# Performance work log

Measured on AMD Instinct MI355X. Metric: run time of the kernel, lower is better.

## Reference

```python
import jax, jax.numpy as jnp
import numpy as np
from jax import lax

TAU_REF_HOURS = 1.0
INIT_NOISE_SCALE = 0.01
MAX_GROWTH_RATE = 0.3
B, T, N, D = 2, 64, 512, 256


def setup_inputs() -> dict:
    key = jax.random.key(0)
    ks = jax.random.split(key, 8)
    return {
        "x": jax.random.normal(ks[0], (B, T, N, D), dtype=jnp.float32),
        "dt": jax.random.uniform(ks[1], (B, T), dtype=jnp.float32),
        "eps": jax.random.normal(ks[2], (B, T, N, D), dtype=jnp.float32),
        "u_raw_re": jax.random.normal(ks[3], (D, D), dtype=jnp.float32) * 0.02,
        "u_raw_im": jax.random.normal(ks[4], (D, D), dtype=jnp.float32) * 0.02,
        "lam_re": jax.random.normal(ks[5], (D,), dtype=jnp.float32) * 0.01,
        "lam_im": jax.random.normal(ks[6], (D,), dtype=jnp.float32) * 0.1,
        "noise_raw": jax.random.normal(ks[7], (D,), dtype=jnp.float32) * 0.02,
    }


def reference(x, dt, eps, u_raw_re, u_raw_im, lam_re, lam_im, noise_raw):
    # Unitary basis from QR of complex raw matrix (ComplexSVDTransform._unitary_from_raw)
    u, _ = jnp.linalg.qr(lax.complex(u_raw_re, u_raw_im))  # [D, D] complex

    # encode: x @ conj(u)
    x_enc = jnp.einsum("btnd,de->btne", x.astype(jnp.complex64), jnp.conj(u))

    # effective lambda: lam_re -> -softplus(-lam_re), clamped at -max_growth_rate
    lam_r = jnp.maximum(-jax.nn.softplus(-lam_re), -MAX_GROWTH_RATE)
    lam = lax.complex(lam_r, lam_im)  # [D]

    # continuous decay / forcing operators per (b, t, d)
    exp_arg = (dt / TAU_REF_HOURS)[..., None] * lam  # [B, T, D]
    decay = jnp.exp(exp_arg)
    lam_safe = lam + (1e-8 * jnp.sign(lam_r + 1e-12)).astype(lam.dtype)
    forcing = (decay - 1.0) / lam_safe  # expm1(arg)/lam_safe

    # SDE noise: eps * sqrt(dt) * softplus(noise_raw) * init_noise_scale
    dt_scale = jnp.sqrt(jnp.maximum(dt, 0.0))[:, :, None, None]  # [B,T,1,1]
    n_scale = jax.nn.softplus(noise_raw) * INIT_NOISE_SCALE  # [D]
    noise = eps.astype(jnp.complex64) * (dt_scale * n_scale).astype(jnp.complex64)

    # linear recurrence h_t = decay_t * h_{t-1} + forcing_t * x_enc_t + noise_t
    b_term = forcing[:, :, None, :] * x_enc + noise  # [B,T,N,D]
    a_term = jnp.broadcast_to(decay[:, :, None, :], b_term.shape)

    def combine(e1, e2):
        a1, b1 = e1
        a2, b2 = e2
        return (a2 * a1, a2 * b1 + b2)

    _, h = lax.associative_scan(combine, (a_term, b_term), axis=1)  # [B,T,N,D]

    # decode: h @ u
    y = jnp.einsum("btnd,de->btne", h, u)
    return jnp.stack([y.real, y.imag])  # [2,B,T,N,D] float32
```

## Files before the change

### kernel.cpp

```cpp
#include <hip/hip_runtime.h>
#include <math.h>

#define B_ 2
#define T_ 64
#define N_ 512
#define D_ 256
#define M_ (B_*T_*N_)
#define PLANE ((size_t)M_*D_)

typedef unsigned short u16;
typedef __attribute__((ext_vector_type(8))) short bf16x8;
typedef __attribute__((ext_vector_type(4))) float f32x4;

__device__ __forceinline__ u16 f2bf(float f) {
  union { float f; unsigned u; } cv; cv.f = f;
  unsigned u = cv.u;
  return (u16)((u + 0x7FFFu + ((u >> 16) & 1u)) >> 16);
}
__device__ __forceinline__ float bf2f(u16 h) {
  union { unsigned u; float f; } cv; cv.u = ((unsigned)h) << 16;
  return cv.f;
}

__device__ __forceinline__ float wredsum(float x) {
  x += __uint_as_float(__builtin_amdgcn_update_dpp(0u, __float_as_uint(x), 0x111, 0xf, 0xf, true));
  x += __uint_as_float(__builtin_amdgcn_update_dpp(0u, __float_as_uint(x), 0x112, 0xf, 0xf, true));
  x += __uint_as_float(__builtin_amdgcn_update_dpp(0u, __float_as_uint(x), 0x114, 0xf, 0xf, true));
  x += __uint_as_float(__builtin_amdgcn_update_dpp(0u, __float_as_uint(x), 0x118, 0xf, 0xf, true));
  x += __uint_as_float(__builtin_amdgcn_update_dpp(0u, __float_as_uint(x), 0x142, 0xa, 0xf, true));
  x += __uint_as_float(__builtin_amdgcn_update_dpp(0u, __float_as_uint(x), 0x143, 0xc, 0xf, true));
  return __uint_as_float(__builtin_amdgcn_readlane(__float_as_uint(x), 63));
}
__device__ __forceinline__ float lanebcast(float x, int l) {
  return __uint_as_float(__builtin_amdgcn_readlane(__float_as_uint(x), l));
}

template<int P>
__global__ __launch_bounds__(1024, 1) void qr_megastep(
    const float* __restrict__ ure_raw, const float* __restrict__ uim_raw,
    float2* __restrict__ A, float2* __restrict__ tau)
{
  const int tid = threadIdx.x, lane = tid & 63, w = tid >> 6;
  const int role = blockIdx.x;
  __shared__ float2 sv32[32][256];
  __shared__ float2 sfin[32][256];
  __shared__ float2 snA[2][256];
  __shared__ float2 snB[2][256];
  __shared__ float4 sscalAB[2];
  __shared__ float2 sg[2];
  __shared__ float2 stau32[32];
  __shared__ float2 stauOut[32];

  constexpr int J0P  = (P > 0) ? 32*(P-1) : 0;
  constexpr int RP   = 256 - J0P;
  constexpr int MCHP = (RP + 63) >> 6;
  constexpr int PIV  = (P == 0) ? 0 : 32;
  constexpr int J0W  = (P == 0) ? 0 : J0P;
  constexpr int RW   = 256 - J0W;
  constexpr int MCHW = (RW + 63) >> 6;

  if constexpr (P == 0) {
    if (role > 0) {
      const int c0 = 32*role;
      const int c = tid & 31, r0 = tid >> 5;
      #pragma unroll
      for (int r8 = 0; r8 < 8; ++r8) {
        int r = r0 + r8*32;
        A[(size_t)(c0+c)*D_ + r] = make_float2(ure_raw[(size_t)r*D_ + c0 + c],
                                               uim_raw[(size_t)r*D_ + c0 + c]);
      }
      return;
    }
  }

  float2 col[2][4];

  if constexpr (P > 0) {
    #pragma unroll
    for (int it = 0; it < 8; ++it) {
      int idx = it*1024 + tid;
      int c = idx >> 8, rr = idx & 255;
      float2 val = make_float2(0.f, 0.f);
      if (rr < RP) val = A[(size_t)(J0P+c)*D_ + J0P + rr];
      sv32[c][rr] = val;
    }
    if (tid < 32) stau32[tid] = tau[J0P + tid];
    const int c0 = (role > 0) ? 32*(P + role) : 32*P;
    #pragma unroll
    for (int lc = 0; lc < 2; ++lc) {
      int cg = c0 + 2*w + lc;
      #pragma unroll
      for (int m = 0; m < 4; ++m) {
        int rr = m*64 + lane;
        col[lc][m] = make_float2(0.f, 0.f);
        if (m < MCHP && rr < RP) col[lc][m] = A[(size_t)cg*D_ + J0P + rr];
      }
    }
    __syncthreads();

    #pragma unroll 4
    for (int jl = 0; jl < 32; ++jl) {
      float2 tt = stau32[jl];
      float2 v[4];
      { float2 rv = sv32[jl][lane];
        v[0] = (lane > jl) ? rv : ((lane == jl) ? make_float2(1.f, 0.f)
                                                : make_float2(0.f, 0.f)); }
      #pragma unroll
      for (int m = 1; m < 4; ++m) v[m] = sv32[jl][m*64 + lane];
      float wr[2], wi[2];
      #pragma unroll
      for (int lc = 0; lc < 2; ++lc) {
        wr[lc] = 0.f; wi[lc] = 0.f;
        #pragma unroll
        for (int m = 0; m < 4; ++m) {
          if (m < MCHP) {
            float2 a = col[lc][m];
            wr[lc] += v[m].x*a.x + v[m].y*a.y;
            wi[lc] += v[m].x*a.y - v[m].y*a.x;
          }
        }
      }
      #pragma unroll
      for (int lc = 0; lc < 2; ++lc) { wr[lc] = wredsum(wr[lc]);
                                       wi[lc] = wredsum(wi[lc]); }
      #pragma unroll
      for (int lc = 0; lc < 2; ++lc) {
        float fr = tt.x*wr[lc] + tt.y*wi[lc];
        float fi = tt.x*wi[lc] - tt.y*wr[lc];
        #pragma unroll
        for (int m = 0; m < 4; ++m) {
          if (m < MCHP) {
            col[lc][m].x -= fr*v[m].x - fi*v[m].y;
            col[lc][m].y -= fr*v[m].y + fi*v[m].x;
          }
        }
      }
    }

    if (role > 0) {
      #pragma unroll
      for (int lc = 0; lc < 2; ++lc) {
        int cg = 32*(P + role) + 2*w + lc;
        #pragma unroll
        for (int m = 0; m < 4; ++m) {
          int rr = m*64 + lane;
          if (m < MCHP && rr < RP) A[(size_t)cg*D_ + J0P + rr] = col[lc][m];
        }
      }
      return;
    }
    __syncthreads();
  } else {
    #pragma unroll
    for (int lc = 0; lc < 2; ++lc) {
      int cg = 2*w + lc;
      #pragma unroll
      for (int m = 0; m < 4; ++m) {
        int rr = m*64 + lane;
        col[lc][m] = make_float2(ure_raw[(size_t)rr*D_ + cg],
                                 uim_raw[(size_t)rr*D_ + cg]);
      }
    }
  }

  auto derive_pair = [&](float2 (&ca)[4], float2 (&cb)[4], int jlA, int buf) {
    const int prA = PIV + jlA, prB = prA + 1;
    float part = (lane > prA) ? (ca[0].x*ca[0].x + ca[0].y*ca[0].y) : 0.f;
    if (1 < MCHW) part += ca[1].x*ca[1].x + ca[1].y*ca[1].y;
    if (2 < MCHW) part += ca[2].x*ca[2].x + ca[2].y*ca[2].y;
    if (3 < MCHW) part += ca[3].x*ca[3].x + ca[3].y*ca[3].y;
    part = wredsum(part);
    float ar = lanebcast(ca[0].x, prA), ai = lanebcast(ca[0].y, prA);
    float trA, tiA, sr, si, btA;
    if (part == 0.f && ai == 0.f) {
      trA = tiA = sr = si = 0.f; btA = ar;
    } else {
      float nrm = sqrtf(ar*ar + ai*ai + part);
      btA = (ar >= 0.f) ? -nrm : nrm;
      trA = (btA - ar)/btA; tiA = -ai/btA;
      float dr = ar - btA, di = ai, dn = dr*dr + di*di;
      sr = dr/dn; si = -di/dn;
    }
    float2 vA[4];
    {
      float2 t0 = make_float2(ca[0].x*sr - ca[0].y*si, ca[0].x*si + ca[0].y*sr);
      vA[0] = (lane > prA) ? t0 : ((lane == prA) ? make_float2(1.f, 0.f)
                                                 : make_float2(0.f, 0.f));
    }
    vA[1] = make_float2(ca[1].x*sr - ca[1].y*si, ca[1].x*si + ca[1].y*sr);
    vA[2] = make_float2(ca[2].x*sr - ca[2].y*si, ca[2].x*si + ca[2].y*sr);
    vA[3] = make_float2(ca[3].x*sr - ca[3].y*si, ca[3].x*si + ca[3].y*sr);
    {
      float2 o0 = (lane < prA) ? ca[0]
                : ((lane == prA) ? make_float2(btA, 0.f) : vA[0]);
      sfin[jlA][lane] = o0;
      if (1 < MCHW) sfin[jlA][64 + lane]  = vA[1];
      if (2 < MCHW) sfin[jlA][128 + lane] = vA[2];
      if (3 < MCHW) sfin[jlA][192 + lane] = vA[3];
    }
    {
      float wr_ = vA[0].x*cb[0].x + vA[0].y*cb[0].y;
      float wi_ = vA[0].x*cb[0].y - vA[0].y*cb[0].x;
      if (1 < MCHW) { wr_ += vA[1].x*cb[1].x + vA[1].y*cb[1].y;
                      wi_ += vA[1].x*cb[1].y - vA[1].y*cb[1].x; }
      if (2 < MCHW) { wr_ += vA[2].x*cb[2].x + vA[2].y*cb[2].y;
                      wi_ += vA[2].x*cb[2].y - vA[2].y*cb[2].x; }
      if (3 < MCHW) { wr_ += vA[3].x*cb[3].x + vA[3].y*cb[3].y;
                      wi_ += vA[3].x*cb[3].y - vA[3].y*cb[3].x; }
      wr_ = wredsum(wr_); wi_ = wredsum(wi_);
      float fr = trA*wr_ + tiA*wi_;
      float fi = trA*wi_ - tiA*wr_;
      cb[0].x -= fr*vA[0].x - fi*vA[0].y; cb[0].y -= fr*vA[0].y + fi*vA[0].x;
      if (1 < MCHW) { cb[1].x -= fr*vA[1].x - fi*vA[1].y;
                      cb[1].y -= fr*vA[1].y + fi*vA[1].x; }
      if (2 < MCHW) { cb[2].x -= fr*vA[2].x - fi*vA[2].y;
                      cb[2].y -= fr*vA[2].y + fi*vA[2].x; }
      if (3 < MCHW) { cb[3].x -= fr*vA[3].x - fi*vA[3].y;
                      cb[3].y -= fr*vA[3].y + fi*vA[3].x; }
    }
    float partB = (lane > prB) ? (cb[0].x*cb[0].x + cb[0].y*cb[0].y) : 0.f;
    if (1 < MCHW) partB += cb[1].x*cb[1].x + cb[1].y*cb[1].y;
    if (2 < MCHW) partB += cb[2].x*cb[2].x + cb[2].y*cb[2].y;
    if (3 < MCHW) partB += cb[3].x*cb[3].x + cb[3].y*cb[3].y;
    partB = wredsum(partB);
    float br_ = lanebcast(cb[0].x, prB), bi_ = lanebcast(cb[0].y, prB);
    float trB, tiB, srB, siB, btB;
    if (partB == 0.f && bi_ == 0.f) {
      trB = tiB = srB = siB = 0.f; btB = br_;
    } else {
      float nrm = sqrtf(br_*br_ + bi_*bi_ + partB);
      btB = (br_ >= 0.f) ? -nrm : nrm;
      trB = (btB - br_)/btB; tiB = -bi_/btB;
      float dr = br_ - btB, di = bi_, dn = dr*dr + di*di;
      srB = dr/dn; siB = -di/dn;
    }
    float2 vB[4];
    {
      float2 t0 = make_float2(cb[0].x*srB - cb[0].y*siB, cb[0].x*siB + cb[0].y*srB);
      vB[0] = (lane > prB) ? t0 : ((lane == prB) ? make_float2(1.f, 0.f)
                                                 : make_float2(0.f, 0.f));
    }
    vB[1] = make_float2(cb[1].x*srB - cb[1].y*siB, cb[1].x*siB + cb[1].y*srB);
    vB[2] = make_float2(cb[2].x*srB - cb[2].y*siB, cb[2].x*siB + cb[2].y*srB);
    vB[3] = make_float2(cb[3].x*srB - cb[3].y*siB, cb[3].x*siB + cb[3].y*srB);
    {
      float2 o0 = (lane < prB) ? cb[0]
                : ((lane == prB) ? make_float2(btB, 0.f) : vB[0]);
      sfin[jlA+1][lane] = o0;
      if (1 < MCHW) sfin[jlA+1][64 + lane]  = vB[1];
      if (2 < MCHW) sfin[jlA+1][128 + lane] = vB[2];
      if (3 < MCHW) sfin[jlA+1][192 + lane] = vB[3];
    }
    float gr = vB[0].x*vA[0].x + vB[0].y*vA[0].y;
    float gi = vB[0].x*vA[0].y - vB[0].y*vA[0].x;
    if (1 < MCHW) { gr += vB[1].x*vA[1].x + vB[1].y*vA[1].y;
                    gi += vB[1].x*vA[1].y - vB[1].y*vA[1].x; }
    if (2 < MCHW) { gr += vB[2].x*vA[2].x + vB[2].y*vA[2].y;
                    gi += vB[2].x*vA[2].y - vB[2].y*vA[2].x; }
    if (3 < MCHW) { gr += vB[3].x*vA[3].x + vB[3].y*vA[3].y;
                    gi += vB[3].x*vA[3].y - vB[3].y*vA[3].x; }
    gr = wredsum(gr); gi = wredsum(gi);
    snA[buf][lane] = vA[0]; snA[buf][64+lane] = vA[1];
    snA[buf][128+lane] = vA[2]; snA[buf][192+lane] = vA[3];
    snB[buf][lane] = vB[0]; snB[buf][64+lane] = vB[1];
    snB[buf][128+lane] = vB[2]; snB[buf][192+lane] = vB[3];
    if (lane == 0) {
      sscalAB[buf] = make_float4(trA, tiA, trB, tiB);
      sg[buf] = make_float2(gr, gi);
      stauOut[jlA]   = make_float2(trA, tiA);
      stauOut[jlA+1] = make_float2(trB, tiB);
    }
  };

  if (w == 0) derive_pair(col[0], col[1], 0, 0);
  __syncthreads();

  #pragma unroll 1
  for (int m = 0; m < 15; ++m) {
    const int cur = m & 1, nxt = cur ^ 1;
    float2 vA0 = snA[cur][lane],       vA1 = snA[cur][64 + lane],
           vA2 = snA[cur][128 + lane], vA3 = snA[cur][192 + lane];
    float2 vB0 = snB[cur][lane],       vB1 = snB[cur][64 + lane],
           vB2 = snB[cur][128 + lane], vB3 = snB[cur][192 + lane];
    float4 sc = sscalAB[cur];
    float2 g  = sg[cur];
    #pragma unroll
    for (int lc = 0; lc < 2; ++lc) {
      int cl = 2*w + lc;
      if (cl > 2*m + 1) {
        float d1r, d1i, d2r, d2i;
        { float2 a = col[lc][0];
          d1r = vA0.x*a.x + vA0.y*a.y; d1i = vA0.x*a.y - vA0.y*a.x;
          d2r = vB0.x*a.x + vB0.y*a.y; d2i = vB0.x*a.y - vB0.y*a.x; }
        if (1 < MCHW) { float2 a = col[lc][1];
          d1r += vA1.x*a.x + vA1.y*a.y; d1i += vA1.x*a.y - vA1.y*a.x;
          d2r += vB1.x*a.x + vB1.y*a.y; d2i += vB1.x*a.y - vB1.y*a.x; }
        if (2 < MCHW) { float2 a = col[lc][2];
          d1r += vA2.x*a.x + vA2.y*a.y; d1i += vA2.x*a.y - vA2.y*a.x;
          d2r += vB2.x*a.x + vB2.y*a.y; d2i += vB2.x*a.y - vB2.y*a.x; }
        if (3 < MCHW) { float2 a = col[lc][3];
          d1r += vA3.x*a.x + vA3.y*a.y; d1i += vA3.x*a.y - vA3.y*a.x;
          d2r += vB3.x*a.x + vB3.y*a.y; d2i += vB3.x*a.y - vB3.y*a.x; }
        d1r = wredsum(d1r); d1i = wredsum(d1i);
        d2r = wredsum(d2r); d2i = wredsum(d2i);
        float f1r = sc.x*d1r + sc.y*d1i;
        float f1i = sc.x*d1i - sc.y*d1r;
        float d2cr = d2r - (f1r*g.x - f1i*g.y);
        float d2ci = d2i - (f1r*g.y + f1i*g.x);
        float f2r = sc.z*d2cr + sc.w*d2ci;
        float f2i = sc.z*d2ci - sc.w*d2cr;
        { col[lc][0].x -= f1r*vA0.x - f1i*vA0.y + f2r*vB0.x - f2i*vB0.y;
          col[lc][0].y -= f1r*vA0.y + f1i*vA0.x + f2r*vB0.y + f2i*vB0.x; }
        if (1 < MCHW) {
          col[lc][1].x -= f1r*vA1.x - f1i*vA1.y + f2r*vB1.x - f2i*vB1.y;
          col[lc][1].y -= f1r*vA1.y + f1i*vA1.x + f2r*vB1.y + f2i*vB1.x; }
        if (2 < MCHW) {
          col[lc][2].x -= f1r*vA2.x - f1i*vA2.y + f2r*vB2.x - f2i*vB2.y;
          col[lc][2].y -= f1r*vA2.y + f1i*vA2.x + f2r*vB2.y + f2i*vB2.x; }
        if (3 < MCHW) {
          col[lc][3].x -= f1r*vA3.x - f1i*vA3.y + f2r*vB3.x - f2i*vB3.y;
          col[lc][3].y -= f1r*vA3.y + f1i*vA3.x + f2r*vB3.y + f2i*vB3.x; }
      }
    }
    if (w == m + 1) derive_pair(col[0], col[1], 2*m + 2, nxt);
    __syncthreads();
  }

  #pragma unroll
  for (int it = 0; it < 8; ++it) {
    int idx = it*1024 + tid;
    int c = idx >> 8, rr = idx & 255;
    if (rr < RW) A[(size_t)(32*P + c)*D_ + J0W + rr] = sfin[c][rr];
  }
  if (tid < 32) tau[32*P + tid] = stauOut[tid];
}

__global__ __launch_bounds__(256, 1) void qr_bwd_kernel(
    const float2* __restrict__ A, const float2* __restrict__ tau,
    u16* __restrict__ Benc, u16* __restrict__ Bdec)
{
  const int lane = threadIdx.x & 63;
  const int w = threadIdx.x >> 6;
  const int c = blockIdx.x * 4 + w;
  __shared__ float2 stau[256];
  if (threadIdx.x < 256) stau[threadIdx.x] = tau[threadIdx.x];
  __syncthreads();

  float2 q[4];
  #pragma unroll
  for (int m = 0; m < 4; ++m) {
    q[m] = make_float2(0.f, 0.f);
    if (m*64 + lane == c) q[m].x = 1.f;
  }
  float2 A0[4], A1[4], A2[4], A3[4];
  {
    int i0 = c, i1 = (c >= 1) ? c-1 : 0, i2 = (c >= 2) ? c-2 : 0,
        i3 = (c >= 3) ? c-3 : 0;
    #pragma unroll
    for (int m = 0; m < 4; ++m) {
      A0[m] = A[(size_t)i0*D_ + m*64 + lane];
      A1[m] = A[(size_t)i1*D_ + m*64 + lane];
      A2[m] = A[(size_t)i2*D_ + m*64 + lane];
      A3[m] = A[(size_t)i3*D_ + m*64 + lane];
    }
  }

  int i = c;
  #pragma unroll 1
  while (i >= 1) {
    float2 ta = stau[i], tb = stau[i-1];
    float2 vI[4], vJ[4];
    #pragma unroll
    for (int m = 0; m < 4; ++m) {
      int r = m*64 + lane;
      vI[m] = (r > i)   ? A0[m] : ((r == i)   ? make_float2(1.f, 0.f)
                                              : make_float2(0.f, 0.f));
      vJ[m] = (r > i-1) ? A1[m] : ((r == i-1) ? make_float2(1.f, 0.f)
                                              : make_float2(0.f, 0.f));
    }
    float2 P0[4], P1[4];
    {
      int n0 = (i >= 4) ? i-4 : 0, n1 = (i >= 5) ? i-5 : 0;
      #pragma unroll
      for (int m = 0; m < 4; ++m) {
        P0[m] = A[(size_t)n0*D_ + m*64 + lane];
        P1[m] = A[(size_t)n1*D_ + m*64 + lane];
      }
    }
    float d1r = 0.f, d1i = 0.f, d2r = 0.f, d2i = 0.f, gr = 0.f, gi = 0.f;
    #pragma unroll
    for (int m = 0; m < 4; ++m) {
      d1r += vI[m].x*q[m].x + vI[m].y*q[m].y;
      d1i += vI[m].x*q[m].y - vI[m].y*q[m].x;
      d2r += vJ[m].x*q[m].x + vJ[m].y*q[m].y;
      d2i += vJ[m].x*q[m].y - vJ[m].y*q[m].x;
      gr  += vJ[m].x*vI[m].x + vJ[m].y*vI[m].y;
      gi  += vJ[m].x*vI[m].y - vJ[m].y*vI[m].x;
    }
    d1r = wredsum(d1r); d1i = wredsum(d1i);
    d2r = wredsum(d2r); d2i = wredsum(d2i);
    gr  = wredsum(gr);  gi  = wredsum(gi);
    float f1r = ta.x*d1r - ta.y*d1i;
    float f1i = ta.x*d1i + ta.y*d1r;
    float d2cr = d2r - (f1r*gr - f1i*gi);
    float d2ci = d2i - (f1r*gi + f1i*gr);
    float f2r = tb.x*d2cr - tb.y*d2ci;
    float f2i = tb.x*d2ci + tb.y*d2cr;
    #pragma unroll
    for (int m = 0; m < 4; ++m) {
      q[m].x -= f1r*vI[m].x - f1i*vI[m].y + f2r*vJ[m].x - f2i*vJ[m].y;
      q[m].y -= f1r*vI[m].y + f1i*vI[m].x + f2r*vJ[m].y + f2i*vJ[m].x;
      A0[m] = A2[m]; A1[m] = A3[m]; A2[m] = P0[m]; A3[m] = P1[m];
    }
    i -= 2;
  }
  if (i == 0) {
    float2 tt = stau[0];
    float2 v0[4];
    #pragma unroll
    for (int m = 0; m < 4; ++m) {
      int r = m*64 + lane;
      v0[m] = (r > 0) ? A0[m] : make_float2(1.f, 0.f);
    }
    float wr = 0.f, wi = 0.f;
    #pragma unroll
    for (int m = 0; m < 4; ++m) {
      wr += v0[m].x*q[m].x + v0[m].y*q[m].y;
      wi += v0[m].x*q[m].y - v0[m].y*q[m].x;
    }
    wr = wredsum(wr); wi = wredsum(wi);
    float fr = tt.x*wr - tt.y*wi;
    float fi = tt.x*wi + tt.y*wr;
    #pragma unroll
    for (int m = 0; m < 4; ++m) {
      q[m].x -= fr*v0[m].x - fi*v0[m].y;
      q[m].y -= fr*v0[m].y + fi*v0[m].x;
    }
  }

  #pragma unroll
  for (int m = 0; m < 4; ++m) {
    int r = m*64 + lane;
    u16 qre = f2bf(q[m].x), qim = f2bf(q[m].y), qimn = f2bf(-q[m].y);
    Benc[(size_t)c*D_ + r]              = qre;
    Benc[(size_t)(c+256)*D_ + r]        = qim;
    Bdec[(size_t)c*512 + r]             = qre;
    Bdec[(size_t)c*512 + 256 + r]       = qimn;
    Bdec[(size_t)(c+256)*512 + r]       = qim;
    Bdec[(size_t)(c+256)*512 + 256 + r] = qre;
  }
}

__global__ __launch_bounds__(256) void coef_kernel(
  const float* __restrict__ dt, const float* __restrict__ lam_re, const float* __restrict__ lam_im,
  const float* __restrict__ noise_raw,
  float* __restrict__ c_dre, float* __restrict__ c_dim, float* __restrict__ c_fre,
  float* __restrict__ c_fim, float* __restrict__ c_ns)
{
  int bt = blockIdx.x; int d = threadIdx.x;
  float dtv = dt[bt];
  float lr = lam_re[d], li = lam_im[d];
  float lam_r = fmaxf(-log1pf(expf(-lr)), -0.3f);
  float ar = dtv*lam_r, ai = dtv*li;
  float er = expf(ar);
  float dre = er*cosf(ai), dim_ = er*sinf(ai);
  float t = lam_r + 1e-12f;
  float sgn = (t > 0.f) ? 1.f : ((t < 0.f) ? -1.f : 0.f);
  float den_re = lam_r + 1e-8f*sgn, den_im = li;
  float nr = dre - 1.f, ni = dim_;
  float d2 = den_re*den_re + den_im*den_im;
  float fre = (nr*den_re + ni*den_im)/d2;
  float fim = (ni*den_re - nr*den_im)/d2;
  float ns = sqrtf(fmaxf(dtv,0.f)) * log1pf(expf(noise_raw[d])) * 0.01f;
  int idx = bt*D_+d;
  c_dre[idx]=dre; c_dim[idx]=dim_; c_fre[idx]=fre; c_fim[idx]=fim; c_ns[idx]=ns;
}

#define LDT 72

__device__ __forceinline__ void gemm_tile_idx(int bid, int& m0, int& n0) {
  int ml = bid & 7, t = bid >> 3;
  int n = t & 3, mg = t >> 2;
  m0 = (mg*8 + ml)*128;
  n0 = n*128;
}

__global__ __launch_bounds__(256) void encode_gemm(
    const float* __restrict__ x, const u16* __restrict__ Bt,
    u16* __restrict__ xer16, u16* __restrict__ xei16)
{
  __shared__ u16 sA[128*LDT];
  __shared__ u16 sB[128*LDT];
  const int tid = threadIdx.x;
  const int lane = tid & 63, w = tid >> 6;
  const int wr = w >> 1, wc = w & 1;
  const int l15 = lane & 15, l4 = lane >> 4;
  int m0, n0;
  gemm_tile_idx(blockIdx.x, m0, n0);
  f32x4 acc[4][4] = {};
  for (int kb = 0; kb < 4; ++kb) {
    #pragma unroll
    for (int i = 0; i < 4; ++i) {
      int chunk = i*256 + tid;
      int row = chunk >> 3, k0 = (chunk & 7) * 8;
      const float* xs = x + (size_t)(m0+row)*D_ + kb*64 + k0;
      float4 f0 = *(const float4*)xs;
      float4 f1 = *(const float4*)(xs + 4);
      int4 va;
      va.x = (int)((unsigned)f2bf(f0.x) | ((unsigned)f2bf(f0.y) << 16));
      va.y = (int)((unsigned)f2bf(f0.z) | ((unsigned)f2bf(f0.w) << 16));
      va.z = (int)((unsigned)f2bf(f1.x) | ((unsigned)f2bf(f1.y) << 16));
      va.w = (int)((unsigned)f2bf(f1.z) | ((unsigned)f2bf(f1.w) << 16));
      int4 vb = *(const int4*)(Bt + (size_t)(n0+row)*D_ + kb*64 + k0);
      *(int4*)&sA[row*LDT + k0] = va;
      *(int4*)&sB[row*LDT + k0] = vb;
    }
    __syncthreads();
    #pragma unroll
    for (int ks = 0; ks < 2; ++ks) {
      bf16x8 af[4], bb[4];
      #pragma unroll
      for (int mf = 0; mf < 4; ++mf)
        af[mf] = *(const bf16x8*)&sA[(wr*64 + mf*16 + l15)*LDT + ks*32 + l4*8];
      #pragma unroll
      for (int nf = 0; nf < 4; ++nf)
        bb[nf] = *(const bf16x8*)&sB[(wc*64 + nf*16 + l15)*LDT + ks*32 + l4*8];
      #pragma unroll
      for (int mf = 0; mf < 4; ++mf)
        #pragma unroll
        for (int nf = 0; nf < 4; ++nf)
          acc[mf][nf] = __builtin_amdgcn_mfma_f32_16x16x32_bf16(
              af[mf], bb[nf], acc[mf][nf], 0, 0, 0);
    }
    __syncthreads();
  }
  #pragma unroll
  for (int mf = 0; mf < 4; ++mf)
    #pragma unroll
    for (int nf = 0; nf < 4; ++nf)
      #pragma unroll
      for (int r = 0; r < 4; ++r) {
        int row = m0 + wr*64 + mf*16 + l4*4 + r;
        int col = n0 + wc*64 + nf*16 + l15;
        float v = acc[mf][nf][r];
        if (col < 256) xer16[(size_t)row*D_ + col] = f2bf(v);
        else           xei16[(size_t)row*D_ + col - 256] = f2bf(-v);
      }
}

__global__ __launch_bounds__(256) void decode_gemm(
    const u16* __restrict__ hre16, const u16* __restrict__ him16,
    const u16* __restrict__ Bt, float* __restrict__ out)
{
  __shared__ u16 sA[128*LDT];
  __shared__ u16 sB[128*LDT];
  const int tid = threadIdx.x;
  const int lane = tid & 63, w = tid >> 6;
  const int wr = w >> 1, wc = w & 1;
  const int l15 = lane & 15, l4 = lane >> 4;
  int m0, n0;
  gemm_tile_idx(blockIdx.x, m0, n0);
  f32x4 acc[4][4] = {};
  for (int kb = 0; kb < 8; ++kb) {
    const u16* aplane = (kb < 4) ? hre16 : him16;
    const int kk = (kb & 3) * 64;
    #pragma unroll
    for (int i = 0; i < 4; ++i) {
      int chunk = i*256 + tid;
      int row = chunk >> 3, k0 = (chunk & 7) * 8;
      int4 va = *(const int4*)(aplane + (size_t)(m0+row)*D_ + kk + k0);
      int4 vb = *(const int4*)(Bt + (size_t)(n0+row)*512 + kb*64 + k0);
      *(int4*)&sA[row*LDT + k0] = va;
      *(int4*)&sB[row*LDT + k0] = vb;
    }
    __syncthreads();
    #pragma unroll
    for (int ks = 0; ks < 2; ++ks) {
      bf16x8 af[4], bb[4];
      #pragma unroll
      for (int mf = 0; mf < 4; ++mf)
        af[mf] = *(const bf16x8*)&sA[(wr*64 + mf*16 + l15)*LDT + ks*32 + l4*8];
      #pragma unroll
      for (int nf = 0; nf < 4; ++nf)
        bb[nf] = *(const bf16x8*)&sB[(wc*64 + nf*16 + l15)*LDT + ks*32 + l4*8];
      #pragma unroll
      for (int mf = 0; mf < 4; ++mf)
        #pragma unroll
        for (int nf = 0; nf < 4; ++nf)
          acc[mf][nf] = __builtin_amdgcn_mfma_f32_16x16x32_bf16(
              af[mf], bb[nf], acc[mf][nf], 0, 0, 0);
    }
    __syncthreads();
  }
  #pragma unroll
  for (int mf = 0; mf < 4; ++mf)
    #pragma unroll
    for (int nf = 0; nf < 4; ++nf)
      #pragma unroll
      for (int r = 0; r < 4; ++r) {
        int row = m0 + wr*64 + mf*16 + l4*4 + r;
        int col = n0 + wc*64 + nf*16 + l15;
        float v = acc[mf][nf][r];
        if (col < 256) out[(size_t)row*D_ + col] = v;
        else           out[PLANE + (size_t)row*D_ + col - 256] = v;
      }
}

__global__ __launch_bounds__(256) void scan_kernel(
  const float* __restrict__ eps,
  const float* __restrict__ c_dre, const float* __restrict__ c_dim,
  const float* __restrict__ c_fre, const float* __restrict__ c_fim, const float* __restrict__ c_ns,
  const u16* __restrict__ xer16, const u16* __restrict__ xei16,
  u16* __restrict__ hre16, u16* __restrict__ him16)
{
  int bx = blockIdx.x;
  int b = bx >> 9, n = bx & 511;
  int d = threadIdx.x;
  float hr = 0.f, hi = 0.f;
  for (int t = 0; t < T_; ++t) {
    int bt = b*T_ + t;
    int cidx = bt*D_ + d;
    float dre = c_dre[cidx], dim_ = c_dim[cidx];
    float fre = c_fre[cidx], fim = c_fim[cidx];
    float ns  = c_ns[cidx];
    size_t idx = ((size_t)bt*N_ + n)*D_ + d;
    float xr = bf2f(xer16[idx]), xi = bf2f(xei16[idx]), ep = eps[idx];
    float br = fre*xr - fim*xi + ep*ns;
    float bi = fre*xi + fim*xr;
    float nr2 = dre*hr - dim_*hi + br;
    float ni2 = dre*hi + dim_*hr + bi;
    hr = nr2; hi = ni2;
    hre16[idx] = f2bf(hr); him16[idx] = f2bf(hi);
  }
}

extern "C" void kernel_launch(void* const* d_in, const int* in_sizes, int n_in,
                              void* d_out, int out_size, void* d_ws, size_t ws_size,
                              hipStream_t stream)
{
  const float* x         = (const float*)d_in[0];
  const float* dt        = (const float*)d_in[1];
  const float* eps       = (const float*)d_in[2];
  const float* ure_raw   = (const float*)d_in[3];
  const float* uim_raw   = (const float*)d_in[4];
  const float* lam_re    = (const float*)d_in[5];
  const float* lam_im    = (const float*)d_in[6];
  const float* noise_raw = (const float*)d_in[7];
  float* out = (float*)d_out;

  char* ws = (char*)d_ws;
  float2* A    = (float2*)(ws);
  float2* tau  = (float2*)(ws + 524288);
  u16* Benc    = (u16*)(ws + (1<<20));
  u16* Bdec    = (u16*)(ws + 1572864);
  float* c_dre = (float*)(ws + (2<<20));
  float* c_dim = c_dre + B_*T_*D_;
  float* c_fre = c_dim + B_*T_*D_;
  float* c_fim = c_fre + B_*T_*D_;
  float* c_ns  = c_fim + B_*T_*D_;
  u16* hre16   = (u16*)(ws + ((size_t)4<<20));
  u16* xer16   = (u16*)(ws + ((size_t)36<<20));
  u16* xei16   = (u16*)(ws + ((size_t)68<<20));
  u16* him16   = (u16*)(ws + ((size_t)100<<20));

  qr_megastep<0><<<8, 1024, 0, stream>>>(ure_raw, uim_raw, A, tau);
  qr_megastep<1><<<7, 1024, 0, stream>>>(ure_raw, uim_raw, A, tau);
  qr_megastep<2><<<6, 1024, 0, stream>>>(ure_raw, uim_raw, A, tau);
  qr_megastep<3><<<5, 1024, 0, stream>>>(ure_raw, uim_raw, A, tau);
  qr_megastep<4><<<4, 1024, 0, stream>>>(ure_raw, uim_raw, A, tau);
  qr_megastep<5><<<3, 1024, 0, stream>>>(ure_raw, uim_raw, A, tau);
  qr_megastep<6><<<2, 1024, 0, stream>>>(ure_raw, uim_raw, A, tau);
  qr_megastep<7><<<1, 1024, 0, stream>>>(ure_raw, uim_raw, A, tau);
  qr_bwd_kernel<<<64, 256, 0, stream>>>(A, tau, Benc, Bdec);
  coef_kernel<<<B_*T_, 256, 0, stream>>>(dt, lam_re, lam_im, noise_raw,
                                         c_dre, c_dim, c_fre, c_fim, c_ns);
  encode_gemm<<<2048, 256, 0, stream>>>(x, Benc, xer16, xei16);
  scan_kernel<<<B_*N_, 256, 0, stream>>>(eps, c_dre, c_dim, c_fre, c_fim, c_ns,
                                         xer16, xei16, hre16, him16);
  decode_gemm<<<2048, 256, 0, stream>>>(hre16, him16, Bdec, out);
}
```

Baseline: 709.1 us.

## Apply Householder reflectors in pairs using precomputed Gram inner products

Each warp first computes the inner product between consecutive Householder vectors (v_b^H v_a) and stores it in shared memory. The trailing-column update then applies two reflectors per iteration: it computes both dot products against the unmodified column, corrects the second coefficient with the Gram term, and performs a single combined rank-2 update. This halves the serial chain of dependent wave reductions and column updates in the QR panel application. The cost is an extra sync and prologue pass, plus slightly different floating-point rounding.

```diff
diff --git a/kernel.cpp b/kernel.cpp
--- a/kernel.cpp
+++ b/kernel.cpp
@@ -48,6 +48,7 @@
   __shared__ float2 snB[2][256];
   __shared__ float4 sscalAB[2];
   __shared__ float2 sg[2];
+  __shared__ float2 sgp[16];
   __shared__ float2 stau32[32];
   __shared__ float2 stauOut[32];
 
@@ -98,40 +99,74 @@
     }
     __syncthreads();
 
-    #pragma unroll 4
-    for (int jl = 0; jl < 32; ++jl) {
-      float2 tt = stau32[jl];
-      float2 v[4];
-      { float2 rv = sv32[jl][lane];
-        v[0] = (lane > jl) ? rv : ((lane == jl) ? make_float2(1.f, 0.f)
-                                                : make_float2(0.f, 0.f)); }
-      #pragma unroll
-      for (int m = 1; m < 4; ++m) v[m] = sv32[jl][m*64 + lane];
-      float wr[2], wi[2];
+    {
+      const int ja = 2*w, jb = 2*w + 1;
+      float2 va[4], vb[4];
+      { float2 rv = sv32[ja][lane];
+        va[0] = (lane > ja) ? rv : ((lane == ja) ? make_float2(1.f, 0.f)
+                                                 : make_float2(0.f, 0.f)); }
+      { float2 rv = sv32[jb][lane];
+        vb[0] = (lane > jb) ? rv : ((lane == jb) ? make_float2(1.f, 0.f)
+                                                 : make_float2(0.f, 0.f)); }
+      #pragma unroll
+      for (int m = 1; m < 4; ++m) { va[m] = sv32[ja][m*64 + lane];
+                                    vb[m] = sv32[jb][m*64 + lane]; }
+      float gr = 0.f, gi = 0.f;
+      #pragma unroll
+      for (int m = 0; m < 4; ++m) {
+        if (m < MCHP) {
+          gr += vb[m].x*va[m].x + vb[m].y*va[m].y;
+          gi += vb[m].x*va[m].y - vb[m].y*va[m].x;
+        }
+      }
+      gr = wredsum(gr); gi = wredsum(gi);
+      if (lane == 0) sgp[w] = make_float2(gr, gi);
+    }
+    __syncthreads();
+
+    #pragma unroll 2
+    for (int m = 0; m < 16; ++m) {
+      const int ja = 2*m, jb = 2*m + 1;
+      float2 tA = stau32[ja], tB = stau32[jb];
+      float2 g = sgp[m];
+      float2 vA[4], vB[4];
+      { float2 rv = sv32[ja][lane];
+        vA[0] = (lane > ja) ? rv : ((lane == ja) ? make_float2(1.f, 0.f)
+                                                 : make_float2(0.f, 0.f)); }
+      { float2 rv = sv32[jb][lane];
+        vB[0] = (lane > jb) ? rv : ((lane == jb) ? make_float2(1.f, 0.f)
+                                                 : make_float2(0.f, 0.f)); }
+      #pragma unroll
+      for (int mm = 1; mm < 4; ++mm) { vA[mm] = sv32[ja][mm*64 + lane];
+                                       vB[mm] = sv32[jb][mm*64 + lane]; }
       #pragma unroll
       for (int lc = 0; lc < 2; ++lc) {
-        wr[lc] = 0.f; wi[lc] = 0.f;
+        float d1r = 0.f, d1i = 0.f, d2r = 0.f, d2i = 0.f;
         #pragma unroll
-        for (int m = 0; m < 4; ++m) {
-          if (m < MCHP) {
-            float2 a = col[lc][m];
-            wr[lc] += v[m].x*a.x + v[m].y*a.y;
-            wi[lc] += v[m].x*a.y - v[m].y*a.x;
+        for (int mm = 0; mm < 4; ++mm) {
+          if (mm < MCHP) {
+            float2 a = col[lc][mm];
+            d1r += vA[mm].x*a.x + vA[mm].y*a.y;
+            d1i += vA[mm].x*a.y - vA[mm].y*a.x;
+            d2r += vB[mm].x*a.x + vB[mm].y*a.y;
+            d2i += vB[mm].x*a.y - vB[mm].y*a.x;
           }
         }
-      }
-      #pragma unroll
-      for (int lc = 0; lc < 2; ++lc) { wr[lc] = wredsum(wr[lc]);
-                                       wi[lc] = wredsum(wi[lc]); }
-      #pragma unroll
-      for (int lc = 0; lc < 2; ++lc) {
-        float fr = tt.x*wr[lc] + tt.y*wi[lc];
-        float fi = tt.x*wi[lc] - tt.y*wr[lc];
+        d1r = wredsum(d1r); d1i = wredsum(d1i);
+        d2r = wredsum(d2r); d2i = wredsum(d2i);
+        float f1r = tA.x*d1r + tA.y*d1i;
+        float f1i = tA.x*d1i - tA.y*d1r;
+        float d2cr = d2r - (f1r*g.x - f1i*g.y);
+        float d2ci = d2i - (f1r*g.y + f1i*g.x);
+        float f2r = tB.x*d2cr + tB.y*d2ci;
+        float f2i = tB.x*d2ci - tB.y*d2cr;
         #pragma unroll
-        for (int m = 0; m < 4; ++m) {
-          if (m < MCHP) {
-            col[lc][m].x -= fr*v[m].x - fi*v[m].y;
-            col[lc][m].y -= fr*v[m].y + fi*v[m].x;
+        for (int mm = 0; mm < 4; ++mm) {
+          if (mm < MCHP) {
+            col[lc][mm].x -= f1r*vA[mm].x - f1i*vA[mm].y
+                           + f2r*vB[mm].x - f2i*vB[mm].y;
+            col[lc][mm].y -= f1r*vA[mm].y + f1i*vA[mm].x
+                           + f2r*vB[mm].y + f2i*vB[mm].x;
           }
         }
       }
```

New measurement: 712.1 us. Within noise of the previous version (+0.4%).
